# Kernel tuning notes

Hardware: AMD Instinct MI355X
Metric: run time of the kernel (lower is better)

## Reference

```python
import jax, jax.numpy as jnp
import numpy as np

B, S = 4, 4096
D_MODEL = 64
D_GENE = 16
N_HEADS = 4
D_HEAD_QK = 16  # d_model//n_heads * head_expand(=1.0)
D_HEAD_V = 16   # d_model // n_heads


def setup_inputs() -> dict:
    key = jax.random.key(0)
    ks = jax.random.split(key, 6)
    x = jax.random.normal(ks[0], (B, S, D_MODEL), dtype=jnp.float32)
    gene_id = jax.random.normal(ks[1], (B, S, D_GENE), dtype=jnp.float32)
    qk_in = D_MODEL + D_GENE
    sq = 1.0 / np.sqrt(qk_in)
    sv = 1.0 / np.sqrt(D_MODEL)
    so = 1.0 / np.sqrt(N_HEADS * D_HEAD_V)
    # weights stored [in, out] (transpose of torch nn.Linear layout)
    Wq = jax.random.uniform(ks[2], (qk_in, N_HEADS * D_HEAD_QK), jnp.float32, -sq, sq)
    Wk = jax.random.uniform(ks[3], (qk_in, N_HEADS * D_HEAD_QK), jnp.float32, -sq, sq)
    Wv = jax.random.uniform(ks[4], (D_MODEL, N_HEADS * D_HEAD_V), jnp.float32, -sv, sv)
    Wo = jax.random.uniform(ks[5], (N_HEADS * D_HEAD_V, D_MODEL), jnp.float32, -so, so)
    return {"x": x, "gene_id": gene_id, "Wq": Wq, "Wk": Wk, "Wv": Wv, "Wo": Wo}


def reference(x, gene_id, Wq, Wk, Wv, Wo):
    b, s, _ = x.shape
    x_id = jnp.concatenate([x, gene_id], axis=-1)            # [B,S,d_model+d_gene]
    q = (x_id @ Wq).reshape(b, s, N_HEADS, D_HEAD_QK)
    k = (x_id @ Wk).reshape(b, s, N_HEADS, D_HEAD_QK)
    v = (x @ Wv).reshape(b, s, N_HEADS, D_HEAD_V)
    scale = D_HEAD_QK ** -0.5
    attn = jnp.einsum('bqhd,bkhd->bhqk', q, k) * scale       # [B,H,S,S]
    attn = jax.nn.softmax(attn, axis=-1)                     # attn_dropout=0.0 -> identity
    out = jnp.einsum('bhqk,bkhd->bqhd', attn, v)             # [B,S,H,Dv]
    out = out.reshape(b, s, N_HEADS * D_HEAD_V)
    return out @ Wo
```

## Files before the change

### kernel.cpp

```cpp
#include <hip/hip_runtime.h>

#define S_LEN 4096

typedef __attribute__((ext_vector_type(4)))  float f32x4;
typedef __attribute__((ext_vector_type(16))) float f32x16;
typedef __attribute__((ext_vector_type(8)))  short bf16x8;
typedef __attribute__((ext_vector_type(4)))  short bf16x4;
typedef __attribute__((ext_vector_type(4)))  unsigned short us4;

static __device__ __forceinline__ unsigned short f2bf(float f) {
    unsigned u = __float_as_uint(f);
    return (unsigned short)((u + 0x7fffu + ((u >> 16) & 1u)) >> 16);
}

static __device__ __forceinline__ float fast_exp2(float x) {
#if __has_builtin(__builtin_amdgcn_exp2f)
    return __builtin_amdgcn_exp2f(x);
#else
    return exp2f(x);
#endif
}

__global__ __launch_bounds__(256) void ga_proj(
    const float* __restrict__ x, const float* __restrict__ gene,
    const float* __restrict__ Wq, const float* __restrict__ Wk,
    const float* __restrict__ Wv,
    unsigned short* __restrict__ Qw, unsigned short* __restrict__ Kw,
    unsigned short* __restrict__ VTw)
{
    __shared__ __align__(16) unsigned short wfrag[6][5][64][8];

    const int tid = threadIdx.x;
    const int tok0 = blockIdx.x * 128;
    const int b = tok0 >> 12;
    const int s0 = tok0 & 4095;

    for (int idx = tid; idx < 80 * 64; idx += 256) {
        int k = idx >> 6, c = idx & 63;
        float w = Wq[idx] * 0.36067376022224085f;
        wfrag[c >> 5][k >> 4][(((k >> 3) & 1) << 5) | (c & 31)][k & 7] = f2bf(w);
    }
    for (int idx = tid; idx < 80 * 64; idx += 256) {
        int k = idx >> 6, c = idx & 63;
        int cg = c + 64;
        wfrag[cg >> 5][k >> 4][(((k >> 3) & 1) << 5) | (c & 31)][k & 7] = f2bf(Wk[idx]);
    }
    for (int idx = tid; idx < 64 * 64; idx += 256) {
        int k = idx >> 6, c = idx & 63;
        int cg = c + 128;
        wfrag[cg >> 5][k >> 4][(((k >> 3) & 1) << 5) | (c & 31)][k & 7] = f2bf(Wv[idx]);
    }
    for (int idx = tid; idx < 1024; idx += 256) {
        int nt = 4 + (idx >> 9);
        int rest = idx & 511;
        wfrag[nt][4][rest >> 3][rest & 7] = 0;
    }
    __syncthreads();

    const int lane = tid & 63;
    const int wave = tid >> 6;
    const int lq = lane & 31, hi = lane >> 5;
    const int tok = tok0 + wave * 32 + lq;

    bf16x8 afrag[5];
    #pragma unroll
    for (int kk = 0; kk < 4; ++kk) {
        const float* p = x + (size_t)tok * 64 + kk * 16 + hi * 8;
        float4 l4 = *(const float4*)p;
        float4 h4 = *(const float4*)(p + 4);
        bf16x8 av;
        av[0] = (short)f2bf(l4.x); av[1] = (short)f2bf(l4.y);
        av[2] = (short)f2bf(l4.z); av[3] = (short)f2bf(l4.w);
        av[4] = (short)f2bf(h4.x); av[5] = (short)f2bf(h4.y);
        av[6] = (short)f2bf(h4.z); av[7] = (short)f2bf(h4.w);
        afrag[kk] = av;
    }
    {
        const float* p = gene + (size_t)tok * 16 + hi * 8;
        float4 l4 = *(const float4*)p;
        float4 h4 = *(const float4*)(p + 4);
        bf16x8 av;
        av[0] = (short)f2bf(l4.x); av[1] = (short)f2bf(l4.y);
        av[2] = (short)f2bf(l4.z); av[3] = (short)f2bf(l4.w);
        av[4] = (short)f2bf(h4.x); av[5] = (short)f2bf(h4.y);
        av[6] = (short)f2bf(h4.z); av[7] = (short)f2bf(h4.w);
        afrag[4] = av;
    }

    const f32x16 z16 = {};
    #pragma unroll
    for (int nt = 0; nt < 6; ++nt) {
        f32x16 acc = z16;
        #pragma unroll
        for (int kk = 0; kk < 5; ++kk) {
            bf16x8 bfr = *(const bf16x8*)&wfrag[nt][kk][lane][0];
            acc = __builtin_amdgcn_mfma_f32_32x32x16_bf16(afrag[kk], bfr, acc, 0, 0, 0);
        }
        const int c = nt * 32 + lq;
        if (nt < 2) {
            int h = c >> 4, d = c & 15;
            size_t base = ((size_t)(b * 4 + h) * S_LEN) * 16 + d;
            #pragma unroll
            for (int r = 0; r < 16; ++r) {
                int m = (r & 3) + 8 * (r >> 2) + 4 * hi;
                Qw[base + (size_t)(s0 + wave * 32 + m) * 16] = f2bf(acc[r]);
            }
        } else if (nt < 4) {
            int cc = c - 64;
            int h = cc >> 4, d = cc & 15;
            size_t base = ((size_t)(b * 4 + h) * S_LEN) * 16 + d;
            #pragma unroll
            for (int r = 0; r < 16; ++r) {
                int m = (r & 3) + 8 * (r >> 2) + 4 * hi;
                Kw[base + (size_t)(s0 + wave * 32 + m) * 16] = f2bf(acc[r]);
            }
        } else {
            int vc = c - 128;
            size_t vbase = ((size_t)(b * 4 + (vc >> 4)) * 16 + (vc & 15)) * S_LEN;
            #pragma unroll
            for (int g = 0; g < 4; ++g) {
                int m0 = 8 * g + 4 * hi;
                us4 pv = { f2bf(acc[4 * g + 0]), f2bf(acc[4 * g + 1]),
                           f2bf(acc[4 * g + 2]), f2bf(acc[4 * g + 3]) };
                *(us4*)(VTw + vbase + s0 + wave * 32 + m0) = pv;
            }
        }
    }
}

__global__ __launch_bounds__(256) void ga_attn(
    const unsigned short* __restrict__ Qw, const unsigned short* __restrict__ Kw,
    const unsigned short* __restrict__ VTw, float* __restrict__ Ow)
{
    __shared__ __align__(16) unsigned short Pl[4][2][32][44];
    __shared__ float dnl[4][32];

    const int tid = threadIdx.x;
    const int lane = tid & 63;
    const int wave = tid >> 6;
    const int bh = blockIdx.x >> 5;
    const int qt = (blockIdx.x & 31) * 4 + wave;
    const int qbase = qt * 32;
    const int lq = lane & 31, hi = lane >> 5;

    const size_t head = (size_t)bh * S_LEN * 16;
    const bf16x8 qf = *(const bf16x8*)(Qw + head + (size_t)(qbase + lq) * 16 + hi * 8);
    const unsigned short* kp = Kw + head + (size_t)lq * 16 + hi * 8;
    const unsigned short* vp = VTw + head + (size_t)(lane & 15) * S_LEN + (lane >> 4) * 8;
    unsigned short* pw = &Pl[wave][0][lq][4 * hi];
    const unsigned short* pr0 = &Pl[wave][0][lane & 15][(lane >> 4) * 8];
    const unsigned short* pr1 = pr0 + 16 * 44;

    const f32x16 zero16 = {};
    f32x4 acc0 = {}, acc1 = {};
    float denomA = 0.f, denomB = 0.f;

    bf16x8 kf = *(const bf16x8*)(kp);
    bf16x8 vf = *(const bf16x8*)(vp);

    for (int kt = 0; kt < 128; ++kt) {
        f32x16 sv = __builtin_amdgcn_mfma_f32_32x32x16_bf16(kf, qf, zero16, 0, 0, 0);
        bf16x8 vc = vf;
        const int ktn = (kt + 1) & 127;
        kf = *(const bf16x8*)(kp + (size_t)ktn * 512);
        vf = *(const bf16x8*)(vp + (size_t)ktn * 32);

        const int boff = (kt & 1) * (32 * 44);
        #pragma unroll
        for (int g = 0; g < 4; ++g) {
            float p0 = fast_exp2(sv[4*g+0]);
            float p1 = fast_exp2(sv[4*g+1]);
            float p2 = fast_exp2(sv[4*g+2]);
            float p3 = fast_exp2(sv[4*g+3]);
            if (g & 1) denomB += (p0 + p1) + (p2 + p3);
            else       denomA += (p0 + p1) + (p2 + p3);
            us4 pk = { f2bf(p0), f2bf(p1), f2bf(p2), f2bf(p3) };
            *(us4*)(pw + boff + 8 * g) = pk;
        }
        asm volatile("s_waitcnt lgkmcnt(0)" ::: "memory");

        bf16x4 a0l = *(const bf16x4*)(pr0 + boff);
        bf16x4 a0h = *(const bf16x4*)(pr0 + boff + 4);
        bf16x4 a1l = *(const bf16x4*)(pr1 + boff);
        bf16x4 a1h = *(const bf16x4*)(pr1 + boff + 4);
        bf16x8 a0 = __builtin_shufflevector(a0l, a0h, 0,1,2,3,4,5,6,7);
        bf16x8 a1 = __builtin_shufflevector(a1l, a1h, 0,1,2,3,4,5,6,7);
        acc0 = __builtin_amdgcn_mfma_f32_16x16x32_bf16(a0, vc, acc0, 0, 0, 0);
        acc1 = __builtin_amdgcn_mfma_f32_16x16x32_bf16(a1, vc, acc1, 0, 0, 0);
    }

    float denom = denomA + denomB;
    denom += __shfl_xor(denom, 32);
    if (lane < 32) dnl[wave][lane] = denom;
    asm volatile("s_waitcnt lgkmcnt(0)" ::: "memory");

    const int b = bh >> 2, h = bh & 3;
    const int d = lane & 15;
    const int qr = (lane >> 4) * 4;
    float* op = Ow + ((size_t)b * S_LEN + qbase) * 64 + h * 16 + d;
    #pragma unroll
    for (int r = 0; r < 4; ++r) {
        float dn0 = dnl[wave][qr + r];
        float dn1 = dnl[wave][qr + r + 16];
        op[(size_t)(qr + r) * 64]      = acc0[r] / dn0;
        op[(size_t)(qr + r + 16) * 64] = acc1[r] / dn1;
    }
}

__global__ __launch_bounds__(256) void ga_wo(
    const float* __restrict__ O, const float* __restrict__ Wo,
    float* __restrict__ out)
{
    __shared__ float wl[64][64];
    const int tid = threadIdx.x;
    #pragma unroll
    for (int r = 0; r < 16; ++r) {
        int idx = tid + r * 256;
        wl[idx >> 6][idx & 63] = Wo[idx];
    }
    __syncthreads();
    const int o = tid & 63;
    const int t = blockIdx.x * 4 + (tid >> 6);
    const float* orow = O + (size_t)t * 64;
    float acc = 0.f;
    #pragma unroll
    for (int c4 = 0; c4 < 16; ++c4) {
        float4 ov = *(const float4*)(orow + c4 * 4);
        acc += ov.x * wl[c4*4+0][o];
        acc += ov.y * wl[c4*4+1][o];
        acc += ov.z * wl[c4*4+2][o];
        acc += ov.w * wl[c4*4+3][o];
    }
    out[(size_t)t * 64 + o] = acc;
}

extern "C" void kernel_launch(void* const* d_in, const int* in_sizes, int n_in,
                              void* d_out, int out_size, void* d_ws, size_t ws_size,
                              hipStream_t stream) {
    const float* x    = (const float*)d_in[0];
    const float* gene = (const float*)d_in[1];
    const float* Wq   = (const float*)d_in[2];
    const float* Wk   = (const float*)d_in[3];
    const float* Wv   = (const float*)d_in[4];
    const float* Wo   = (const float*)d_in[5];

    unsigned short* Qw  = (unsigned short*)d_ws;
    unsigned short* Kw  = Qw + (1u << 20);
    unsigned short* VTw = Kw + (1u << 20);
    float* Ow = (float*)((char*)d_ws + 6u * (1u << 20));

    ga_proj<<<128, 256, 0, stream>>>(x, gene, Wq, Wk, Wv, Qw, Kw, VTw);
    ga_attn<<<512, 256, 0, stream>>>(Qw, Kw, VTw, Ow);
    ga_wo<<<4096, 256, 0, stream>>>(Ow, Wo, (float*)d_out);
}
```

Before: 156.4 us.

## Split attention key range across waves and reduce partials in shared memory

Result: faster. 132.1 us (-15.5%).

```diff
diff --git a/kernel.cpp b/kernel.cpp
--- a/kernel.cpp
+++ b/kernel.cpp
@@ -7,6 +7,7 @@
 typedef __attribute__((ext_vector_type(8)))  short bf16x8;
 typedef __attribute__((ext_vector_type(4)))  short bf16x4;
 typedef __attribute__((ext_vector_type(4)))  unsigned short us4;
+typedef __attribute__((ext_vector_type(2)))  unsigned int uint2v;
 
 static __device__ __forceinline__ unsigned short f2bf(float f) {
     unsigned u = __float_as_uint(f);
@@ -19,6 +20,12 @@
 #else
     return exp2f(x);
 #endif
+}
+
+static __device__ __forceinline__ unsigned cvt_pk_bf16(float lo, float hi) {
+    unsigned r;
+    asm("v_cvt_pk_bf16_f32 %0, %1, %2" : "=v"(r) : "v"(lo), "v"(hi));
+    return r;
 }
 
 __global__ __launch_bounds__(256) void ga_proj(
@@ -134,12 +141,13 @@
 {
     __shared__ __align__(16) unsigned short Pl[4][2][32][44];
     __shared__ float dnl[4][32];
+    __shared__ __align__(16) float red[4][64][8];
 
     const int tid = threadIdx.x;
     const int lane = tid & 63;
     const int wave = tid >> 6;
-    const int bh = blockIdx.x >> 5;
-    const int qt = (blockIdx.x & 31) * 4 + wave;
+    const int bh = blockIdx.x >> 7;
+    const int qt = blockIdx.x & 127;
     const int qbase = qt * 32;
     const int lq = lane & 31, hi = lane >> 5;
 
@@ -155,17 +163,18 @@
     f32x4 acc0 = {}, acc1 = {};
     float denomA = 0.f, denomB = 0.f;
 
-    bf16x8 kf = *(const bf16x8*)(kp);
-    bf16x8 vf = *(const bf16x8*)(vp);
-
-    for (int kt = 0; kt < 128; ++kt) {
+    const int kt0 = wave * 32;
+    bf16x8 kf = *(const bf16x8*)(kp + (size_t)kt0 * 512);
+    bf16x8 vf = *(const bf16x8*)(vp + (size_t)kt0 * 32);
+
+    for (int i = 0; i < 32; ++i) {
         f32x16 sv = __builtin_amdgcn_mfma_f32_32x32x16_bf16(kf, qf, zero16, 0, 0, 0);
         bf16x8 vc = vf;
-        const int ktn = (kt + 1) & 127;
+        const int ktn = kt0 + ((i + 1) & 31);
         kf = *(const bf16x8*)(kp + (size_t)ktn * 512);
         vf = *(const bf16x8*)(vp + (size_t)ktn * 32);
 
-        const int boff = (kt & 1) * (32 * 44);
+        const int boff = (i & 1) * (32 * 44);
         #pragma unroll
         for (int g = 0; g < 4; ++g) {
             float p0 = fast_exp2(sv[4*g+0]);
@@ -174,8 +183,8 @@
             float p3 = fast_exp2(sv[4*g+3]);
             if (g & 1) denomB += (p0 + p1) + (p2 + p3);
             else       denomA += (p0 + p1) + (p2 + p3);
-            us4 pk = { f2bf(p0), f2bf(p1), f2bf(p2), f2bf(p3) };
-            *(us4*)(pw + boff + 8 * g) = pk;
+            uint2v pk = { cvt_pk_bf16(p0, p1), cvt_pk_bf16(p2, p3) };
+            *(uint2v*)(pw + boff + 8 * g) = pk;
         }
         asm volatile("s_waitcnt lgkmcnt(0)" ::: "memory");
 
@@ -192,18 +201,30 @@
     float denom = denomA + denomB;
     denom += __shfl_xor(denom, 32);
     if (lane < 32) dnl[wave][lane] = denom;
-    asm volatile("s_waitcnt lgkmcnt(0)" ::: "memory");
-
-    const int b = bh >> 2, h = bh & 3;
-    const int d = lane & 15;
-    const int qr = (lane >> 4) * 4;
-    float* op = Ow + ((size_t)b * S_LEN + qbase) * 64 + h * 16 + d;
-    #pragma unroll
-    for (int r = 0; r < 4; ++r) {
-        float dn0 = dnl[wave][qr + r];
-        float dn1 = dnl[wave][qr + r + 16];
-        op[(size_t)(qr + r) * 64]      = acc0[r] / dn0;
-        op[(size_t)(qr + r + 16) * 64] = acc1[r] / dn1;
+
+    __syncthreads();
+    *(f32x4*)&red[wave][lane][0] = acc0;
+    *(f32x4*)&red[wave][lane][4] = acc1;
+    __syncthreads();
+
+    if (wave == 0) {
+        f32x4 r0 = {}, r1 = {};
+        #pragma unroll
+        for (int w = 0; w < 4; ++w) {
+            r0 += *(const f32x4*)&red[w][lane][0];
+            r1 += *(const f32x4*)&red[w][lane][4];
+        }
+        const int b = bh >> 2, h = bh & 3;
+        const int d = lane & 15;
+        const int qr = (lane >> 4) * 4;
+        float* op = Ow + ((size_t)b * S_LEN + qbase) * 64 + h * 16 + d;
+        #pragma unroll
+        for (int r = 0; r < 4; ++r) {
+            float dn0 = dnl[0][qr+r] + dnl[1][qr+r] + dnl[2][qr+r] + dnl[3][qr+r];
+            float dn1 = dnl[0][qr+r+16] + dnl[1][qr+r+16] + dnl[2][qr+r+16] + dnl[3][qr+r+16];
+            op[(size_t)(qr + r) * 64]      = r0[r] / dn0;
+            op[(size_t)(qr + r + 16) * 64] = r1[r] / dn1;
+        }
     }
 }
 
@@ -250,6 +271,6 @@
     float* Ow = (float*)((char*)d_ws + 6u * (1u << 20));
 
     ga_proj<<<128, 256, 0, stream>>>(x, gene, Wq, Wk, Wv, Qw, Kw, VTw);
-    ga_attn<<<512, 256, 0, stream>>>(Qw, Kw, VTw, Ow);
+    ga_attn<<<2048, 256, 0, stream>>>(Qw, Kw, VTw, Ow);
     ga_wo<<<4096, 256, 0, stream>>>(Ow, Wo, (float*)d_out);
 }
```
